# Kernel tuning notes

Measured on AMD Instinct MI355X. Metric: run time of the kernel, lower is better.

Reference implementation:

```python
import jax, jax.numpy as jnp
import numpy as np

EPS = 1e-5
SLOPE = 0.2


def _conv(x, w, b, stride, pad):
    y = jax.lax.conv_general_dilated(
        x, w, (stride, stride), ((pad, pad), (pad, pad)),
        dimension_numbers=('NCHW', 'OIHW', 'NCHW'))
    return y + b[None, :, None, None]


def _inorm(x):
    m = x.mean(axis=(2, 3), keepdims=True)
    v = x.var(axis=(2, 3), keepdims=True)
    return (x - m) * jax.lax.rsqrt(v + EPS)


def _down(x, w, b, norm):
    y = _conv(x, w, b, 2, 1)
    if norm:
        y = _inorm(y)
    return jax.nn.leaky_relu(y, SLOPE)


def _self_attn(x, wq, bq, wk, bk, wv, bv, gamma):
    B, C, H, W = x.shape
    N = H * W
    q = _conv(x, wq, bq, 1, 0).reshape(B, -1, N)   # (B, C/8, N)
    k = _conv(x, wk, bk, 1, 0).reshape(B, -1, N)
    v = _conv(x, wv, bv, 1, 0).reshape(B, C, N)
    attn = jax.nn.softmax(jnp.einsum('bcn,bcm->bnm', q, k), axis=-1)  # (B,N,N)
    out = jnp.einsum('bcm,bnm->bcn', v, attn).reshape(B, C, H, W)
    return gamma * out + x


def _branch(p, img):
    (w0, b0, w1, b1, w2, b2, wq, bq, wk, bk, wv, bv, gamma, wh, bh) = p
    x = _down(img, w0, b0, norm=False)
    x = _down(x, w1, b1, norm=True)
    x = _self_attn(x, wq, bq, wk, bk, wv, bv, gamma)
    x = _down(x, w2, b2, norm=True)
    return _conv(x, wh, bh, 1, 1)  # head: Conv2d(nf*4, 1, 4, padding=1)


def setup_inputs() -> dict:
    key = jax.random.key(0)
    ks = jax.random.split(key, 20)
    S, B, H = 4, 16, 128
    s = 0.05  # weight scale for numerical stability of softmax energies
    d = {
        'img': jax.random.normal(ks[0], (B, 1, H, H), jnp.float32),
        'stage_idx': jax.random.randint(ks[1], (B,), 0, S, jnp.int32),
        'w0': jax.random.normal(ks[2], (S, 64, 1, 4, 4)) * s,
        'b0': jax.random.normal(ks[3], (S, 64)) * s,
        'w1': jax.random.normal(ks[4], (S, 128, 64, 4, 4)) * s,
        'b1': jax.random.normal(ks[5], (S, 128)) * s,
        'w2': jax.random.normal(ks[6], (S, 256, 128, 4, 4)) * s,
        'b2': jax.random.normal(ks[7], (S, 256)) * s,
        'wq': jax.random.normal(ks[8], (S, 16, 128, 1, 1)) * s,
        'bq': jax.random.normal(ks[9], (S, 16)) * s,
        'wk': jax.random.normal(ks[10], (S, 16, 128, 1, 1)) * s,
        'bk': jax.random.normal(ks[11], (S, 16)) * s,
        'wv': jax.random.normal(ks[12], (S, 128, 128, 1, 1)) * s,
        'bv': jax.random.normal(ks[13], (S, 128)) * s,
        'gamma': jax.random.normal(ks[14], (S,)) * s,
        'wh': jax.random.normal(ks[15], (S, 1, 256, 4, 4)) * s,
        'bh': jax.random.normal(ks[16], (S, 1)) * s,
    }
    return d


def reference(img, stage_idx, w0, b0, w1, b1, w2, b2, wq, bq, wk, bk, wv, bv, gamma, wh, bh):
    params = (w0, b0, w1, b1, w2, b2, wq, bq, wk, bk, wv, bv, gamma, wh, bh)
    # compute every branch for every sample (as the original), stacked over stage axis
    all_preds = jax.vmap(_branch, in_axes=(0, None))(params, img)  # (S, B, 1, h, w)
    B = img.shape[0]
    return all_preds[stage_idx, jnp.arange(B)]  # (B, 1, h, w)
```

## Files before the change

kernel.cpp:

```cpp
#include <hip/hip_runtime.h>

#define LRELU(x) ((x) > 0.0f ? (x) : 0.2f * (x))
#define SB __builtin_amdgcn_sched_barrier(0)

typedef short bf16x8 __attribute__((ext_vector_type(8)));
typedef short bf16x4 __attribute__((ext_vector_type(4)));
typedef float f32x4 __attribute__((ext_vector_type(4)));

__device__ __forceinline__ short f2bf(float f) {
  union { float f; unsigned u; } x{f};
  return (short)((x.u + 0x7FFF + ((x.u >> 16) & 1)) >> 16);
}

__global__ __launch_bounds__(256) void k_repack_all(
    const float* __restrict__ w1, unsigned short* __restrict__ wr1,
    const float* __restrict__ w2, unsigned short* __restrict__ wr2,
    const float* __restrict__ bh, const int* __restrict__ sidx,
    float* __restrict__ out, unsigned short* __restrict__ x0t,
    unsigned short* __restrict__ ybf, const float* __restrict__ img,
    const float* __restrict__ w0, const float* __restrict__ b0) {
  __shared__ float Ish[4 * 34];
  if (blockIdx.x >= 10517) {
    const int t = threadIdx.x;
    const int q = blockIdx.x - 10517;
    const int b = q >> 8, py = q & 255;
    const int oh = py >> 2, owb = (py & 3) << 4;
    const int s = sidx[b];
    const float* ip = img + (size_t)b * 16384;
    if (t < 136) {
      int r = t / 34, c = t % 34;
      int ih = 2 * oh - 1 + r, iw = 2 * owb - 1 + c;
      Ish[t] = ((unsigned)ih < 128u && (unsigned)iw < 128u) ? ip[ih * 128 + iw] : 0.f;
    }
    const int co = t & 63, ps = t >> 6;
    float wreg[16];
    const float* wp = w0 + (s * 64 + co) * 16;
#pragma unroll
    for (int i = 0; i < 16; i++) wreg[i] = wp[i];
    float bb = b0[s * 64 + co];
    __syncthreads();
    unsigned short* op = x0t + ((size_t)b * 4356 + (oh + 1) * 66 + (owb + 1)) * 64 + co;
#pragma unroll
    for (int j = 0; j < 4; j++) {
      int pl = ps * 4 + j;
      float acc = bb;
#pragma unroll
      for (int kh = 0; kh < 4; kh++)
#pragma unroll
        for (int kw = 0; kw < 4; kw++)
          acc += wreg[kh * 4 + kw] * Ish[kh * 34 + pl * 2 + kw];
      acc = LRELU(acc);
      op[pl * 64] = (unsigned short)f2bf(acc);
    }
    return;
  }
  int idx = blockIdx.x * 256 + threadIdx.x;
  if (idx < 524288) {
    int tap = idx & 15;
    int rest = idx >> 4;
    int ci = rest & 63, sco = rest >> 6;
    wr1[(size_t)sco * 1024 + tap * 64 + ci] = (unsigned short)f2bf(w1[idx]);
    return;
  } else if (idx < 2621440) {
    int i = idx - 524288;
    int tap = i & 15;
    int rest = i >> 4;
    int ci = rest & 127, sco = rest >> 7;
    wr2[(size_t)sco * 2048 + tap * 128 + ci] = (unsigned short)f2bf(w2[i]);
    return;
  } else if (idx < 2625040) {
    int i = idx - 2621440;
    if (i < 3600) out[i] = bh[sidx[i / 225]];
    return;
  } else if (idx < 2658320) {
    int i = idx - 2625040;
    int b = i / 2080, r = i % 2080;
    int pix = r >> 3, sub = r & 7;
    int row, col;
    if (pix < 66) { row = 0; col = pix; }
    else if (pix < 132) { row = 65; col = pix - 66; }
    else { int qq = pix - 132; row = 1 + (qq >> 1); col = (qq & 1) * 65; }
    bf16x8 z = {0, 0, 0, 0, 0, 0, 0, 0};
    *(bf16x8*)(x0t + ((size_t)b * 4356 + row * 66 + col) * 64 + sub * 8) = z;
    return;
  } else {
    int i = idx - 2658320;
    if (i >= 33792) return;
    int b = i / 2112, r = i % 2112;
    int pix = r >> 4, sub = r & 15;
    int row, col;
    if (pix < 34) { row = 0; col = pix; }
    else if (pix < 68) { row = 33; col = pix - 34; }
    else { int qq = pix - 68; row = 1 + (qq >> 1); col = (qq & 1) * 33; }
    bf16x8 z = {0, 0, 0, 0, 0, 0, 0, 0};
    *(bf16x8*)(ybf + ((size_t)b * 1156 + row * 34 + col) * 128 + sub * 8) = z;
    return;
  }
}

__global__ __launch_bounds__(256, 2) void k_conv1(
    const unsigned short* __restrict__ xt, const unsigned short* __restrict__ wr,
    const int* __restrict__ sidx, float* __restrict__ out) {
  constexpr int CI = 64, CO = 128;
  constexpr int NPB = 1024, NT = 16;
  const int t = threadIdx.x;
  const int b = blockIdx.x;
  const int co0 = (blockIdx.y / NT) * 64;
  const int n0 = (blockIdx.y % NT) * 64;
  const int s = sidx[b];
  const int lane = t & 63, wv = t >> 6;
  const int wm = (wv >> 1) * 32, wn = (wv & 1) * 32;
  const int quad = lane >> 4, l16 = lane & 15;

  const unsigned short* aptr0 = wr + (size_t)(s * CO + co0 + wm + l16) * (CI * 16) + quad * 8;
  const unsigned short* aptr1 = aptr0 + (size_t)16 * (CI * 16);
  const unsigned short* xb = xt + (size_t)b * 4356 * CI;
  int pb0, pb1;
  {
    int p = n0 + wn + l16;
    pb0 = 2 * (p >> 5) * 66 + 2 * (p & 31);
    p += 16;
    pb1 = 2 * (p >> 5) * 66 + 2 * (p & 31);
  }
  f32x4 acc[2][2];
#pragma unroll
  for (int i = 0; i < 2; i++)
#pragma unroll
    for (int j = 0; j < 2; j++) acc[i][j] = (f32x4){0.f, 0.f, 0.f, 0.f};

  bf16x8 Aaf0[4], Aaf1[4], Abv0[4], Abv1[4];
  bf16x8 Baf0[4], Baf1[4], Bbv0[4], Bbv1[4];

#define LD1(AF0, AF1, BV0, BV1, G)                                            \
  _Pragma("unroll") for (int kk = 0; kk < 4; kk++) {                          \
    int kc = (G) * 4 + kk;                                                    \
    int tap = kc >> 1, cio = (kc & 1) * 32 + quad * 8;                        \
    int kh = tap >> 2, kw = tap & 3;                                          \
    AF0[kk] = *(const bf16x8*)(aptr0 + kc * 32);                              \
    AF1[kk] = *(const bf16x8*)(aptr1 + kc * 32);                              \
    BV0[kk] = *(const bf16x8*)(xb + (size_t)(pb0 + kh * 66 + kw) * CI + cio); \
    BV1[kk] = *(const bf16x8*)(xb + (size_t)(pb1 + kh * 66 + kw) * CI + cio); \
  }                                                                           \
  SB;

#define MM1(AF0, AF1, BV0, BV1)                                                                  \
  _Pragma("unroll") for (int kk = 0; kk < 4; kk++) {                                             \
    acc[0][0] = __builtin_amdgcn_mfma_f32_16x16x32_bf16(AF0[kk], BV0[kk], acc[0][0], 0, 0, 0);   \
    acc[1][0] = __builtin_amdgcn_mfma_f32_16x16x32_bf16(AF1[kk], BV0[kk], acc[1][0], 0, 0, 0);   \
    acc[0][1] = __builtin_amdgcn_mfma_f32_16x16x32_bf16(AF0[kk], BV1[kk], acc[0][1], 0, 0, 0);   \
    acc[1][1] = __builtin_amdgcn_mfma_f32_16x16x32_bf16(AF1[kk], BV1[kk], acc[1][1], 0, 0, 0);   \
  }                                                                                              \
  SB;

  LD1(Aaf0, Aaf1, Abv0, Abv1, 0)
  LD1(Baf0, Baf1, Bbv0, Bbv1, 1)
  MM1(Aaf0, Aaf1, Abv0, Abv1) LD1(Aaf0, Aaf1, Abv0, Abv1, 2)
  MM1(Baf0, Baf1, Bbv0, Bbv1) LD1(Baf0, Baf1, Bbv0, Bbv1, 3)
  MM1(Aaf0, Aaf1, Abv0, Abv1) LD1(Aaf0, Aaf1, Abv0, Abv1, 4)
  MM1(Baf0, Baf1, Bbv0, Bbv1) LD1(Baf0, Baf1, Bbv0, Bbv1, 5)
  MM1(Aaf0, Aaf1, Abv0, Abv1) LD1(Aaf0, Aaf1, Abv0, Abv1, 6)
  MM1(Baf0, Baf1, Bbv0, Bbv1) LD1(Baf0, Baf1, Bbv0, Bbv1, 7)
  MM1(Aaf0, Aaf1, Abv0, Abv1)
  MM1(Baf0, Baf1, Bbv0, Bbv1)
#undef LD1
#undef MM1

#pragma unroll
  for (int i = 0; i < 2; i++) {
    int cobase = co0 + wm + i * 16 + quad * 4;
#pragma unroll
    for (int j = 0; j < 2; j++) {
      int n = n0 + wn + j * 16 + l16;
#pragma unroll
      for (int r = 0; r < 4; r++)
        out[((size_t)b * CO + cobase + r) * NPB + n] = acc[i][j][r];
    }
  }
}

template <int NPIX>
__global__ __launch_bounds__(256) void k_inorm(float* __restrict__ x) {
  constexpr int E = NPIX / 256;
  float* p = x + (size_t)blockIdx.x * NPIX;
  const int t = threadIdx.x;
  float v[E];
  float sum = 0.f, sq = 0.f;
#pragma unroll
  for (int i = 0; i < E; i++) {
    v[i] = p[i * 256 + t];
    sum += v[i];
    sq += v[i] * v[i];
  }
#pragma unroll
  for (int o = 32; o > 0; o >>= 1) {
    sum += __shfl_down(sum, o, 64);
    sq += __shfl_down(sq, o, 64);
  }
  __shared__ float red[8];
  int wid = t >> 6;
  if ((t & 63) == 0) {
    red[wid] = sum;
    red[4 + wid] = sq;
  }
  __syncthreads();
  float S = red[0] + red[1] + red[2] + red[3];
  float SQ = red[4] + red[5] + red[6] + red[7];
  float m = S * (1.0f / NPIX);
  float var = SQ * (1.0f / NPIX) - m * m;
  float inv = rsqrtf(var + 1e-5f);
#pragma unroll
  for (int i = 0; i < E; i++) p[i * 256 + t] = LRELU((v[i] - m) * inv);
}

template <int NPIX>
__global__ __launch_bounds__(256) void k_inormw(float* __restrict__ x) {
  constexpr int E = NPIX / 256;
  const int wv = threadIdx.x >> 6, lane = threadIdx.x & 63;
  const size_t row = (size_t)blockIdx.x * 4 + wv;
  float4* p = (float4*)(x + row * NPIX);
  float4 v[E];
#pragma unroll
  for (int i = 0; i < E; i++) v[i] = p[i * 64 + lane];
  float sum = 0.f, sq = 0.f;
#pragma unroll
  for (int i = 0; i < E; i++) {
    sum += v[i].x + v[i].y + v[i].z + v[i].w;
    sq += v[i].x * v[i].x + v[i].y * v[i].y + v[i].z * v[i].z + v[i].w * v[i].w;
  }
#pragma unroll
  for (int o = 32; o > 0; o >>= 1) {
    sum += __shfl_xor(sum, o, 64);
    sq += __shfl_xor(sq, o, 64);
  }
  float m = sum * (1.0f / NPIX);
  float var = sq * (1.0f / NPIX) - m * m;
  float inv = rsqrtf(var + 1e-5f);
#pragma unroll
  for (int i = 0; i < E; i++) {
    v[i].x = LRELU((v[i].x - m) * inv);
    v[i].y = LRELU((v[i].y - m) * inv);
    v[i].z = LRELU((v[i].z - m) * inv);
    v[i].w = LRELU((v[i].w - m) * inv);
    p[i * 64 + lane] = v[i];
  }
}

__global__ __launch_bounds__(256) void k_proj_qkv(
    const float* __restrict__ xin, const float* __restrict__ wq,
    const float* __restrict__ bq, const float* __restrict__ wk,
    const float* __restrict__ bk, const float* __restrict__ wv,
    const float* __restrict__ bv, const int* __restrict__ sidx,
    float* __restrict__ q, float* __restrict__ kout, unsigned short* __restrict__ vpk) {
  __shared__ float xsh[32 * 256];
  __shared__ float wsh[16 * 32];
  const int t = threadIdx.x;
  const int b = blockIdx.x;
  const int y = blockIdx.y;
  const int s = sidx[b];
  const int cg = t >> 6, ng = t & 63;
  const float* w;
  const float* bias;
  int co0, nn0, CO;
  if (y < 8) {
    w = (y < 4) ? wq : wk;
    bias = (y < 4) ? bq : bk;
    co0 = 0;
    nn0 = (y & 3) * 256;
    CO = 16;
  } else {
    w = wv;
    bias = bv;
    co0 = ((y - 8) >> 2) * 16;
    nn0 = ((y - 8) & 3) * 256;
    CO = 128;
  }
  const float* xb = xin + (size_t)b * 128 * 1024;
  float4 acc4[4];
#pragma unroll
  for (int c = 0; c < 4; c++) {
    float bb = bias[s * CO + co0 + cg * 4 + c];
    acc4[c] = make_float4(bb, bb, bb, bb);
  }
  for (int cc = 0; cc < 4; cc++) {
#pragma unroll
    for (int k = 0; k < 8; k++) {
      int id = t + (k << 8);
      int ci = id >> 6, nf = id & 63;
      ((float4*)xsh)[id] = ((const float4*)(xb + (cc * 32 + ci) * 1024 + nn0))[nf];
    }
    if (t < 128)
      ((float4*)wsh)[t] =
          ((const float4*)(w + ((size_t)(s * CO + co0 + (t >> 3))) * 128 + cc * 32))[t & 7];
    __syncthreads();
#pragma unroll
    for (int ci4 = 0; ci4 < 8; ci4++) {
      float4 wvv[4], xv[4];
#pragma unroll
      for (int c = 0; c < 4; c++) wvv[c] = ((const float4*)wsh)[(cg * 4 + c) * 8 + ci4];
#pragma unroll
      for (int i = 0; i < 4; i++) xv[i] = ((const float4*)xsh)[(ci4 * 4 + i) * 64 + ng];
#pragma unroll
      for (int c = 0; c < 4; c++)
#pragma unroll
        for (int i = 0; i < 4; i++) {
          float wvc = i == 0 ? wvv[c].x : i == 1 ? wvv[c].y : i == 2 ? wvv[c].z : wvv[c].w;
          acc4[c].x += wvc * xv[i].x;
          acc4[c].y += wvc * xv[i].y;
          acc4[c].z += wvc * xv[i].z;
          acc4[c].w += wvc * xv[i].w;
        }
    }
    __syncthreads();
  }
  if (y < 8) {
    float* out = (y < 4) ? q : kout;
#pragma unroll
    for (int c = 0; c < 4; c++)
      ((float4*)(out + ((size_t)b * 16 + cg * 4 + c) * 1024 + nn0))[ng] = acc4[c];
  } else {
    int n = nn0 + ng * 4;
#pragma unroll
    for (int c = 0; c < 4; c++) {
      int co = co0 + cg * 4 + c;
      bf16x4 u;
      u[0] = f2bf(acc4[c].x);
      u[1] = f2bf(acc4[c].y);
      u[2] = f2bf(acc4[c].z);
      u[3] = f2bf(acc4[c].w);
      *(bf16x4*)(vpk + (((size_t)b * 32 + (n >> 5)) * 128 + co) * 32 + (n & 31)) = u;
    }
  }
}

__global__ __launch_bounds__(256, 2) void k_attn(
    const float* __restrict__ q, const float* __restrict__ k,
    const unsigned short* __restrict__ vpk, const float* __restrict__ x1,
    const float* __restrict__ gamma, const int* __restrict__ sidx,
    unsigned short* __restrict__ ybf) {
  __shared__ __align__(16) short Psh[16 * 1032];
  __shared__ float qsh[256];
  __shared__ float redm[64], reds[64];
  const int t = threadIdx.x;
  const int b = blockIdx.x >> 6;
  const int n0 = (blockIdx.x & 63) << 4;
  const int lane = t & 63, wv = t >> 6;
  const int quad = lane >> 4, l16 = lane & 15;
  const float* qb = q + (size_t)b * 16 * 1024;
  const float* kb = k + (size_t)b * 16 * 1024;
  const float* xb = x1 + (size_t)b * 128 * 1024;

  qsh[t] = qb[((t >> 4) << 10) + n0 + (t & 15)];
  __syncthreads();

  float acc[4][16];
#pragma unroll
  for (int j = 0; j < 4; j++)
#pragma unroll
    for (int nl = 0; nl < 16; nl++) acc[j][nl] = 0.0f;

  float4 KA[4], KB[4];
#define LDK(BUF, G)                                                       \
  _Pragma("unroll") for (int c4 = 0; c4 < 4; c4++)                        \
      BUF[c4] = *(const float4*)(kb + ((((G) * 4 + c4)) << 10) + 4 * t);  \
  SB;
#define MMK(BUF, G)                                                                         \
  _Pragma("unroll") for (int c4 = 0; c4 < 4; c4++) {                                        \
    const float* qr = qsh + ((G) * 4 + c4) * 16;                                            \
    _Pragma("unroll") for (int j = 0; j < 4; j++) {                                         \
      float kk = j == 0 ? BUF[c4].x : j == 1 ? BUF[c4].y : j == 2 ? BUF[c4].z : BUF[c4].w;  \
      _Pragma("unroll") for (int nl = 0; nl < 16; nl++) acc[j][nl] += kk * qr[nl];          \
    }                                                                                       \
  }                                                                                         \
  SB;

  LDK(KA, 0)
  LDK(KB, 1)
  MMK(KA, 0) LDK(KA, 2)
  MMK(KB, 1) LDK(KB, 3)
  MMK(KA, 2)
  MMK(KB, 3)
#undef LDK
#undef MMK

  float lmax[16];
#pragma unroll
  for (int nl = 0; nl < 16; nl++)
    lmax[nl] = fmaxf(fmaxf(acc[0][nl], acc[1][nl]), fmaxf(acc[2][nl], acc[3][nl]));
#pragma unroll
  for (int o = 32; o > 0; o >>= 1)
#pragma unroll
    for (int nl = 0; nl < 16; nl++) lmax[nl] = fmaxf(lmax[nl], __shfl_xor(lmax[nl], o, 64));
  if (lane == 0)
#pragma unroll
    for (int nl = 0; nl < 16; nl++) redm[wv * 16 + nl] = lmax[nl];
  __syncthreads();
#pragma unroll
  for (int nl = 0; nl < 16; nl++)
    lmax[nl] = fmaxf(fmaxf(redm[nl], redm[16 + nl]), fmaxf(redm[32 + nl], redm[48 + nl]));
  float lsum[16];
#pragma unroll
  for (int nl = 0; nl < 16; nl++) lsum[nl] = 0.0f;
#pragma unroll
  for (int j = 0; j < 4; j++)
#pragma unroll
    for (int nl = 0; nl < 16; nl++) {
      float e = __expf(acc[j][nl] - lmax[nl]);
      acc[j][nl] = e;
      lsum[nl] += e;
    }
#pragma unroll
  for (int o = 32; o > 0; o >>= 1)
#pragma unroll
    for (int nl = 0; nl < 16; nl++) lsum[nl] += __shfl_xor(lsum[nl], o, 64);
  if (lane == 0)
#pragma unroll
    for (int nl = 0; nl < 16; nl++) reds[wv * 16 + nl] = lsum[nl];
#pragma unroll
  for (int nl = 0; nl < 16; nl++) {
    bf16x4 pv;
    pv[0] = f2bf(acc[0][nl]);
    pv[1] = f2bf(acc[1][nl]);
    pv[2] = f2bf(acc[2][nl]);
    pv[3] = f2bf(acc[3][nl]);
    *(bf16x4*)&Psh[nl * 1032 + 4 * t] = pv;
  }
  __syncthreads();

  const unsigned short* vp =
      vpk + ((size_t)b * 32 * 128 + (size_t)(wv * 32 + l16)) * 32 + quad * 8;
  const short* prow = Psh + l16 * 1032 + quad * 8;
  f32x4 dacc[2];
  dacc[0] = (f32x4){0.f, 0.f, 0.f, 0.f};
  dacc[1] = (f32x4){0.f, 0.f, 0.f, 0.f};

  bf16x8 VA0[4], VA1[4], PAr[4];
  bf16x8 VB0[4], VB1[4], PBr[4];
#define LDV(V0, V1, PR, G)                                \
  _Pragma("unroll") for (int m4 = 0; m4 < 4; m4++) {      \
    int mt = (G) * 4 + m4;                                \
    V0[m4] = *(const bf16x8*)(vp + mt * 4096);            \
    V1[m4] = *(const bf16x8*)(vp + 512 + mt * 4096);      \
    PR[m4] = *(const bf16x8*)(prow + mt * 32);            \
  }                                                       \
  SB;
#define MMV(V0, V1, PR)                                                                      \
  _Pragma("unroll") for (int m4 = 0; m4 < 4; m4++) {                                         \
    dacc[0] = __builtin_amdgcn_mfma_f32_16x16x32_bf16(V0[m4], PR[m4], dacc[0], 0, 0, 0);     \
    dacc[1] = __builtin_amdgcn_mfma_f32_16x16x32_bf16(V1[m4], PR[m4], dacc[1], 0, 0, 0);     \
  }                                                                                          \
  SB;

  LDV(VA0, VA1, PAr, 0)
  LDV(VB0, VB1, PBr, 1)
  MMV(VA0, VA1, PAr) LDV(VA0, VA1, PAr, 2)
  MMV(VB0, VB1, PBr) LDV(VB0, VB1, PBr, 3)
  MMV(VA0, VA1, PAr) LDV(VA0, VA1, PAr, 4)
  MMV(VB0, VB1, PBr) LDV(VB0, VB1, PBr, 5)
  MMV(VA0, VA1, PAr) LDV(VA0, VA1, PAr, 6)
  MMV(VB0, VB1, PBr) LDV(VB0, VB1, PBr, 7)
  MMV(VA0, VA1, PAr)
  MMV(VB0, VB1, PBr)
#undef LDV
#undef MMV
  __syncthreads();

  float* Osh = (float*)Psh;
  short* Osh2 = Psh + 4352;
#pragma unroll
  for (int i = 0; i < 2; i++) {
    int cob = wv * 32 + i * 16 + quad * 4;
#pragma unroll
    for (int r = 0; r < 4; r++) Osh[(cob + r) * 17 + l16] = dacc[i][r];
  }
  __syncthreads();
  float g = gamma[sidx[b]];
  {
    int co = t >> 1, j0 = (t & 1) * 8;
    const float* xr = xb + (co << 10) + n0 + j0;
    float4 xv0 = *(const float4*)xr;
    float4 xv1 = *(const float4*)(xr + 4);
    float xs[8] = {xv0.x, xv0.y, xv0.z, xv0.w, xv1.x, xv1.y, xv1.z, xv1.w};
#pragma unroll
    for (int j = 0; j < 8; j++) {
      int nl = j0 + j;
      float rs = 1.0f / (reds[nl] + reds[16 + nl] + reds[32 + nl] + reds[48 + nl]);
      Osh2[nl * 136 + co] = f2bf(g * Osh[co * 17 + nl] * rs + xs[j]);
    }
  }
  __syncthreads();
  {
    int nl = t >> 4, cg = t & 15;
    bf16x8 u = *(const bf16x8*)&Osh2[nl * 136 + cg * 8];
    int p = n0 + nl;
    int ih = p >> 5, iw = p & 31;
    *(bf16x8*)(ybf + ((size_t)b * 1156 + (ih + 1) * 34 + (iw + 1)) * 128 + cg * 8) = u;
  }
}

__global__ __launch_bounds__(256, 2) void k_conv2n(
    const unsigned short* __restrict__ ybf, const unsigned short* __restrict__ wr,
    const int* __restrict__ sidx, float* __restrict__ x2) {
  __shared__ __align__(16) unsigned short Xs[26624];
  const int t = threadIdx.x;
  const int b = blockIdx.x;
  const int y = blockIdx.y;
  const int ne = y & 7;
  const int cog = y >> 3;
  const int s = sidx[b];
  const int lane = t & 63, wv = t >> 6;
  const int quad = lane >> 4, l16 = lane & 15;

  const unsigned short* gb = ybf + ((size_t)b * 1156 + 4 * ne * 34) * 128;
  {
    float4 v[13];
#pragma unroll
    for (int i = 0; i < 13; i++) v[i] = *(const float4*)(gb + (i * 256 + t) * 8);
#pragma unroll
    for (int i = 0; i < 13; i++) {
      int ba = (i * 256 + t) * 16;
      int sw = ba ^ (((ba >> 9) & 7) << 4);
      *(float4*)((char*)Xs + sw) = v[i];
    }
  }
  __syncthreads();

  const int co0w = cog * 64 + wv * 16;
  const unsigned short* ap = wr + ((size_t)(s * 256 + co0w + l16)) * 2048 + quad * 8;
  f32x4 acc[2];
  acc[0] = (f32x4){0.f, 0.f, 0.f, 0.f};
  acc[1] = (f32x4){0.f, 0.f, 0.f, 0.f};

#pragma unroll
  for (int kc = 0; kc < 64; kc++) {
    const int tap = kc >> 2;
    const int cio = (kc & 3) * 32 + quad * 8;
    const int kh = tap >> 2, kw = tap & 3;
    bf16x8 af = *(const bf16x8*)(ap + kc * 32);
#pragma unroll
    for (int nt = 0; nt < 2; nt++) {
      int lr = 2 * nt + kh;
      int col = 2 * l16 + kw;
      int ba = ((lr * 34 + col) * 128 + cio) * 2;
      int sw = ba ^ (((ba >> 9) & 7) << 4);
      bf16x8 bv = *(const bf16x8*)((const char*)Xs + sw);
      acc[nt] = __builtin_amdgcn_mfma_f32_16x16x32_bf16(af, bv, acc[nt], 0, 0, 0);
    }
  }

#pragma unroll
  for (int nt = 0; nt < 2; nt++) {
    int p = ne * 32 + nt * 16 + l16;
#pragma unroll
    for (int r = 0; r < 4; r++)
      x2[((size_t)b * 256 + co0w + quad * 4 + r) * 256 + p] = acc[nt][r];
  }
}

__global__ __launch_bounds__(256) void k_head_part(
    const float* __restrict__ x2, const float* __restrict__ wh,
    const int* __restrict__ sidx, float* __restrict__ out) {
  __shared__ float Xs[32 * 256];
  __shared__ float Wsh[512];
  const int t = threadIdx.x;
  const int b = blockIdx.x, cc = blockIdx.y;
  const int s = sidx[b];
  const float* xp = x2 + ((size_t)b * 256 + cc * 32) * 256;
#pragma unroll
  for (int i = 0; i < 32; i++) Xs[i * 256 + t] = xp[i * 256 + t];
#pragma unroll
  for (int i = 0; i < 2; i++) {
    int idx = i * 256 + t;
    Wsh[idx] = wh[s * 4096 + cc * 512 + idx];
  }
  __syncthreads();
  if (t < 225) {
    int oh = t / 15, ow = t % 15;
    float acc = 0.0f;
    for (int ci = 0; ci < 32; ci++) {
      const float* xr = Xs + ci * 256;
      const float* wr = Wsh + ci * 16;
#pragma unroll
      for (int kh = 0; kh < 4; kh++) {
        int ih = oh - 1 + kh;
        if ((unsigned)ih >= 16u) continue;
#pragma unroll
        for (int kw = 0; kw < 4; kw++) {
          int iw = ow - 1 + kw;
          if ((unsigned)iw >= 16u) continue;
          acc += wr[kh * 4 + kw] * xr[(ih << 4) + iw];
        }
      }
    }
    atomicAdd(out + b * 225 + t, acc);
  }
}

extern "C" void kernel_launch(void* const* d_in, const int* in_sizes, int n_in,
                              void* d_out, int out_size, void* d_ws, size_t ws_size,
                              hipStream_t stream) {
  const float* img = (const float*)d_in[0];
  const int* sidx = (const int*)d_in[1];
  const float* w0 = (const float*)d_in[2];
  const float* b0 = (const float*)d_in[3];
  const float* w1 = (const float*)d_in[4];
  const float* w2 = (const float*)d_in[6];
  const float* wq = (const float*)d_in[8];
  const float* bq = (const float*)d_in[9];
  const float* wk = (const float*)d_in[10];
  const float* bk = (const float*)d_in[11];
  const float* wv = (const float*)d_in[12];
  const float* bv = (const float*)d_in[13];
  const float* gamma = (const float*)d_in[14];
  const float* wh = (const float*)d_in[15];
  const float* bh = (const float*)d_in[16];
  float* out = (float*)d_out;

  float* ws = (float*)d_ws;
  unsigned short* x0t = (unsigned short*)(ws);
  float* x1 = ws + 2359296;
  float* q = ws + 4456448;
  float* k = ws + 4718592;
  unsigned short* vpk = (unsigned short*)(ws + 4980736);
  unsigned short* ybf = (unsigned short*)(ws + 6029312);
  float* x2 = ws + 7340032;
  unsigned short* wr1 = (unsigned short*)(ws + 8912896);
  unsigned short* wr2 = (unsigned short*)(ws + 9175040);

  const int B = 16;

  k_repack_all<<<14613, 256, 0, stream>>>(w1, wr1, w2, wr2, bh, sidx, out, x0t, ybf,
                                          img, w0, b0);
  k_conv1<<<dim3(B, 32), 256, 0, stream>>>(x0t, wr1, sidx, x1);
  k_inorm<1024><<<B * 128, 256, 0, stream>>>(x1);
  k_proj_qkv<<<dim3(B, 40), 256, 0, stream>>>(x1, wq, bq, wk, bk, wv, bv, sidx, q, k, vpk);
  k_attn<<<B * 64, 256, 0, stream>>>(q, k, vpk, x1, gamma, sidx, ybf);
  k_conv2n<<<dim3(B, 32), 256, 0, stream>>>(ybf, wr2, sidx, x2);
  k_inormw<256><<<1024, 256, 0, stream>>>(x2);
  k_head_part<<<dim3(B, 8), 256, 0, stream>>>(x2, wh, sidx, out);
}
```

Baseline: 224.5 us.

## Stage conv1 input tile in swizzled LDS and reshape warp tiling

The conv1 kernel now copies each block's input halo region (5 padded rows × 66 cols × 64 channels) into shared memory with an XOR swizzle, then reads the B operand of the implicit GEMM from LDS instead of global memory. Each wave now owns 16 output channels across all 64 pixels of the block, rather than a 32x32 tile. The goal is to cut redundant global/L2 loads of overlapping 4x4 stride-2 windows and avoid LDS bank conflicts. In exchange it uses about 52KB of LDS per block, loses the explicit double-buffered register prefetch, and adds a block barrier.

```diff
diff --git a/kernel.cpp b/kernel.cpp
--- a/kernel.cpp
+++ b/kernel.cpp
@@ -98,83 +98,62 @@
   }
 }
 
-__global__ __launch_bounds__(256, 2) void k_conv1(
-    const unsigned short* __restrict__ xt, const unsigned short* __restrict__ wr,
-    const int* __restrict__ sidx, float* __restrict__ out) {
-  constexpr int CI = 64, CO = 128;
-  constexpr int NPB = 1024, NT = 16;
+__global__ __launch_bounds__(256, 2) void k_conv1n(
+    const unsigned short* __restrict__ x0t, const unsigned short* __restrict__ wr,
+    const int* __restrict__ sidx, float* __restrict__ x1) {
+  __shared__ __align__(16) unsigned short Xs[26624];
   const int t = threadIdx.x;
   const int b = blockIdx.x;
-  const int co0 = (blockIdx.y / NT) * 64;
-  const int n0 = (blockIdx.y % NT) * 64;
+  const int y = blockIdx.y;
+  const int ne = y & 15;
+  const int cog = y >> 4;
   const int s = sidx[b];
   const int lane = t & 63, wv = t >> 6;
-  const int wm = (wv >> 1) * 32, wn = (wv & 1) * 32;
   const int quad = lane >> 4, l16 = lane & 15;
 
-  const unsigned short* aptr0 = wr + (size_t)(s * CO + co0 + wm + l16) * (CI * 16) + quad * 8;
-  const unsigned short* aptr1 = aptr0 + (size_t)16 * (CI * 16);
-  const unsigned short* xb = xt + (size_t)b * 4356 * CI;
-  int pb0, pb1;
+  const unsigned short* gb = x0t + ((size_t)b * 4356 + 4 * ne * 66) * 64;
   {
-    int p = n0 + wn + l16;
-    pb0 = 2 * (p >> 5) * 66 + 2 * (p & 31);
-    p += 16;
-    pb1 = 2 * (p >> 5) * 66 + 2 * (p & 31);
-  }
-  f32x4 acc[2][2];
-#pragma unroll
-  for (int i = 0; i < 2; i++)
-#pragma unroll
-    for (int j = 0; j < 2; j++) acc[i][j] = (f32x4){0.f, 0.f, 0.f, 0.f};
-
-  bf16x8 Aaf0[4], Aaf1[4], Abv0[4], Abv1[4];
-  bf16x8 Baf0[4], Baf1[4], Bbv0[4], Bbv1[4];
-
-#define LD1(AF0, AF1, BV0, BV1, G)                                            \
-  _Pragma("unroll") for (int kk = 0; kk < 4; kk++) {                          \
-    int kc = (G) * 4 + kk;                                                    \
-    int tap = kc >> 1, cio = (kc & 1) * 32 + quad * 8;                        \
-    int kh = tap >> 2, kw = tap & 3;                                          \
-    AF0[kk] = *(const bf16x8*)(aptr0 + kc * 32);                              \
-    AF1[kk] = *(const bf16x8*)(aptr1 + kc * 32);                              \
-    BV0[kk] = *(const bf16x8*)(xb + (size_t)(pb0 + kh * 66 + kw) * CI + cio); \
-    BV1[kk] = *(const bf16x8*)(xb + (size_t)(pb1 + kh * 66 + kw) * CI + cio); \
-  }                                                                           \
-  SB;
-
-#define MM1(AF0, AF1, BV0, BV1)                                                                  \
-  _Pragma("unroll") for (int kk = 0; kk < 4; kk++) {                                             \
-    acc[0][0] = __builtin_amdgcn_mfma_f32_16x16x32_bf16(AF0[kk], BV0[kk], acc[0][0], 0, 0, 0);   \
-    acc[1][0] = __builtin_amdgcn_mfma_f32_16x16x32_bf16(AF1[kk], BV0[kk], acc[1][0], 0, 0, 0);   \
-    acc[0][1] = __builtin_amdgcn_mfma_f32_16x16x32_bf16(AF0[kk], BV1[kk], acc[0][1], 0, 0, 0);   \
-    acc[1][1] = __builtin_amdgcn_mfma_f32_16x16x32_bf16(AF1[kk], BV1[kk], acc[1][1], 0, 0, 0);   \
-  }                                                                                              \
-  SB;
-
-  LD1(Aaf0, Aaf1, Abv0, Abv1, 0)
-  LD1(Baf0, Baf1, Bbv0, Bbv1, 1)
-  MM1(Aaf0, Aaf1, Abv0, Abv1) LD1(Aaf0, Aaf1, Abv0, Abv1, 2)
-  MM1(Baf0, Baf1, Bbv0, Bbv1) LD1(Baf0, Baf1, Bbv0, Bbv1, 3)
-  MM1(Aaf0, Aaf1, Abv0, Abv1) LD1(Aaf0, Aaf1, Abv0, Abv1, 4)
-  MM1(Baf0, Baf1, Bbv0, Bbv1) LD1(Baf0, Baf1, Bbv0, Bbv1, 5)
-  MM1(Aaf0, Aaf1, Abv0, Abv1) LD1(Aaf0, Aaf1, Abv0, Abv1, 6)
-  MM1(Baf0, Baf1, Bbv0, Bbv1) LD1(Baf0, Baf1, Bbv0, Bbv1, 7)
-  MM1(Aaf0, Aaf1, Abv0, Abv1)
-  MM1(Baf0, Baf1, Bbv0, Bbv1)
-#undef LD1
-#undef MM1
-
-#pragma unroll
-  for (int i = 0; i < 2; i++) {
-    int cobase = co0 + wm + i * 16 + quad * 4;
-#pragma unroll
-    for (int j = 0; j < 2; j++) {
-      int n = n0 + wn + j * 16 + l16;
-#pragma unroll
-      for (int r = 0; r < 4; r++)
-        out[((size_t)b * CO + cobase + r) * NPB + n] = acc[i][j][r];
-    }
+    float4 v[13];
+#pragma unroll
+    for (int i = 0; i < 13; i++) v[i] = *(const float4*)(gb + (i * 256 + t) * 8);
+#pragma unroll
+    for (int i = 0; i < 13; i++) {
+      int ba = (i * 256 + t) * 16;
+      int sw = ba ^ (((ba >> 9) & 7) << 4);
+      *(float4*)((char*)Xs + sw) = v[i];
+    }
+  }
+  __syncthreads();
+
+  const int co0w = cog * 64 + wv * 16;
+  const unsigned short* ap = wr + ((size_t)(s * 128 + co0w + l16)) * 1024 + quad * 8;
+  f32x4 acc[4];
+#pragma unroll
+  for (int nt = 0; nt < 4; nt++) acc[nt] = (f32x4){0.f, 0.f, 0.f, 0.f};
+
+#pragma unroll
+  for (int kc = 0; kc < 32; kc++) {
+    const int tap = kc >> 1;
+    const int cio = (kc & 1) * 32 + quad * 8;
+    const int kh = tap >> 2, kw = tap & 3;
+    bf16x8 af = *(const bf16x8*)(ap + kc * 32);
+#pragma unroll
+    for (int nt = 0; nt < 4; nt++) {
+      int lr = 2 * (nt >> 1) + kh;
+      int col = 2 * ((nt & 1) * 16 + l16) + kw;
+      int ba = ((lr * 66 + col) * 64 + cio) * 2;
+      int sw = ba ^ (((ba >> 9) & 7) << 4);
+      bf16x8 bv = *(const bf16x8*)((const char*)Xs + sw);
+      acc[nt] = __builtin_amdgcn_mfma_f32_16x16x32_bf16(af, bv, acc[nt], 0, 0, 0);
+    }
+  }
+
+#pragma unroll
+  for (int nt = 0; nt < 4; nt++) {
+    int p = ne * 64 + (nt >> 1) * 32 + (nt & 1) * 16 + l16;
+#pragma unroll
+    for (int r = 0; r < 4; r++)
+      x1[((size_t)b * 128 + co0w + quad * 4 + r) * 1024 + p] = acc[nt][r];
   }
 }
 
@@ -630,7 +609,7 @@
 
   k_repack_all<<<14613, 256, 0, stream>>>(w1, wr1, w2, wr2, bh, sidx, out, x0t, ybf,
                                           img, w0, b0);
-  k_conv1<<<dim3(B, 32), 256, 0, stream>>>(x0t, wr1, sidx, x1);
+  k_conv1n<<<dim3(B, 32), 256, 0, stream>>>(x0t, wr1, sidx, x1);
   k_inorm<1024><<<B * 128, 256, 0, stream>>>(x1);
   k_proj_qkv<<<dim3(B, 40), 256, 0, stream>>>(x1, wq, bq, wk, bk, wv, bv, sidx, q, k, vpk);
   k_attn<<<B * 64, 256, 0, stream>>>(q, k, vpk, x1, gamma, sidx, ybf);
```

Measured after the change: 206.5 us. 1.09x faster.
